# Kernel tuning notes

Measured on AMD Instinct MI355X. Metric: run time of the kernel, lower is better.

Reference implementation:

```python
import jax, jax.numpy as jnp
import numpy as np

B, L, C, H = 4, 2048, 768, 12
D = C // H
MAX_SCALE_MUL = float(np.log(100.0))
BLOCK = 128  # block size for the VAR-style block-causal mask


def _block_causal_bias(L, block):
    # 0 where key-block <= query-block, -inf elsewhere (block lower-triangular)
    bid = np.arange(L) // block
    vis = bid[:, None] >= bid[None, :]
    bias = np.where(vis, 0.0, -np.inf).astype(np.float32)
    return jnp.asarray(bias)[None, None]  # (1,1,L,L)


def setup_inputs() -> dict:
    key = jax.random.key(0)
    ks = jax.random.split(key, 5)
    x = jax.random.normal(ks[0], (B, L, C), dtype=jnp.float32)
    W_qkv = jax.random.normal(ks[1], (3 * C, C), dtype=jnp.float32) * (1.0 / np.sqrt(C))
    q_bias = jnp.zeros((C,), jnp.float32)
    v_bias = jnp.zeros((C,), jnp.float32)
    # module inits scale_mul to log(4.0)
    log_scale_mul = jnp.full((1, H, 1, 1), np.log(4.0), jnp.float32)
    W_proj = jax.random.normal(ks[2], (C, C), dtype=jnp.float32) * (1.0 / np.sqrt(C))
    b_proj = jnp.zeros((C,), jnp.float32)
    attn_bias = _block_causal_bias(L, BLOCK)
    return {"x": x, "attn_bias": attn_bias, "W_qkv": W_qkv, "q_bias": q_bias,
            "v_bias": v_bias, "log_scale_mul": log_scale_mul,
            "W_proj": W_proj, "b_proj": b_proj}


def _l2norm(t, eps=1e-12):
    n = jnp.linalg.norm(t, axis=-1, keepdims=True)
    return t / jnp.maximum(n, eps)


def reference(x, attn_bias, W_qkv, q_bias, v_bias, log_scale_mul, W_proj, b_proj):
    Bx, Lx, Cx = x.shape
    # qkv projection with concatenated (q_bias, zero_k_bias, v_bias)
    bias = jnp.concatenate([q_bias, jnp.zeros_like(q_bias), v_bias])
    qkv = x @ W_qkv.T + bias                      # (B,L,3C)
    qkv = qkv.reshape(Bx, Lx, 3, H, D)
    q, k, v = jnp.moveaxis(qkv, 2, 0)             # each (B,L,H,D)
    q = jnp.swapaxes(q, 1, 2)                     # (B,H,L,D)
    k = jnp.swapaxes(k, 1, 2)
    v = jnp.swapaxes(v, 1, 2)
    # cos-attention: L2-normalize q,k; head-wise learnable scale on q; scale=1
    scale_mul = jnp.exp(jnp.minimum(log_scale_mul, MAX_SCALE_MUL))  # (1,H,1,1)
    q = _l2norm(q) * scale_mul
    k = _l2norm(k)
    scores = jnp.einsum('bhld,bhmd->bhlm', q, k) + attn_bias
    attn = jax.nn.softmax(scores, axis=-1)
    o = jnp.einsum('bhlm,bhmd->bhld', attn, v)    # (B,H,L,D)
    o = jnp.swapaxes(o, 1, 2).reshape(Bx, Lx, Cx)
    return o @ W_proj.T + b_proj
```

## Files before the change

### kernel.cpp

```cpp
#include <hip/hip_runtime.h>
#include <hip/hip_bf16.h>

#define DEV __device__ __forceinline__

typedef __bf16 bf16x8 __attribute__((ext_vector_type(8)));
typedef float  f32x4  __attribute__((ext_vector_type(4)));

typedef __attribute__((address_space(3))) unsigned int LDSU;
typedef __attribute__((address_space(1))) const unsigned int GLBU;

DEV unsigned short f2b(float f){
  __bf16 h = (__bf16)f;
  return __builtin_bit_cast(unsigned short, h);
}

static constexpr float MAXLOG = 4.60517018598809136804f;

__global__ void cvt_kernel(const float4* __restrict__ src, ushort4* __restrict__ dst, int n4){
  int i = blockIdx.x * 256 + threadIdx.x;
  if (i < n4){
    float4 v = src[i];
    ushort4 o;
    o.x = f2b(v.x); o.y = f2b(v.y); o.z = f2b(v.z); o.w = f2b(v.w);
    dst[i] = o;
  }
}

__global__ __launch_bounds__(512) void qkv_gemm(
    const unsigned short* __restrict__ X,
    const unsigned short* __restrict__ W,
    const float* __restrict__ qbias, const float* __restrict__ vbias,
    const float* __restrict__ lsm,
    unsigned short* __restrict__ Qo, unsigned short* __restrict__ Ko,
    unsigned short* __restrict__ Vo)
{
  __shared__ char smem[65536];
  const int tid = threadIdx.x;
  const int l = tid & 63, w = tid >> 6;
  const int wr = w >> 1, wc = w & 1;
  const int lr = l & 15, lg = l >> 4;
  const int tm = blockIdx.x % 64;
  const int tn = blockIdx.x / 64;
  const int m0 = tm * 128, n0 = tn * 128;

  f32x4 acc[2][4];
  #pragma unroll
  for (int i=0;i<2;i++)
    #pragma unroll
    for (int j=0;j<4;j++) acc[i][j] = (f32x4){0.f,0.f,0.f,0.f};

  #pragma unroll
  for (int c=0;c<2;++c){
    int chunk = c*512 + tid;
    int row = chunk >> 3;
    int scc = (chunk & 7) ^ (row & 7);
    __builtin_amdgcn_global_load_lds((GLBU*)(X + (size_t)(m0+row)*768 + scc*8),
                                     (LDSU*)(smem + chunk*16), 16, 0, 0);
    __builtin_amdgcn_global_load_lds((GLBU*)(W + (size_t)(n0+row)*768 + scc*8),
                                     (LDSU*)(smem + 32768 + chunk*16), 16, 0, 0);
  }

  for (int kt = 0; kt < 12; ++kt){
    __syncthreads();
    const int pc = kt & 1;
    char* Acur = smem + pc*16384;
    char* Bcur = smem + 32768 + pc*16384;

    if (kt + 1 < 12){
      const int k1 = (kt+1)*64;
      char* Anxt = smem + (pc^1)*16384;
      char* Bnxt = smem + 32768 + (pc^1)*16384;
      #pragma unroll
      for (int c=0;c<2;++c){
        int chunk = c*512 + tid;
        int row = chunk >> 3;
        int scc = (chunk & 7) ^ (row & 7);
        __builtin_amdgcn_global_load_lds((GLBU*)(X + (size_t)(m0+row)*768 + k1 + scc*8),
                                         (LDSU*)(Anxt + chunk*16), 16, 0, 0);
        __builtin_amdgcn_global_load_lds((GLBU*)(W + (size_t)(n0+row)*768 + k1 + scc*8),
                                         (LDSU*)(Bnxt + chunk*16), 16, 0, 0);
      }
    }

    #pragma unroll
    for (int kk = 0; kk < 2; ++kk){
      bf16x8 af[2], bfv[4];
      #pragma unroll
      for (int m=0;m<2;m++){
        int row = wr*32 + m*16 + lr;
        int byte = kk*64 + lg*16;
        af[m] = *(const bf16x8*)(Acur + row*128 + (byte ^ ((row&7)<<4)));
      }
      #pragma unroll
      for (int n=0;n<4;n++){
        int row = wc*64 + n*16 + lr;
        int byte = kk*64 + lg*16;
        bfv[n] = *(const bf16x8*)(Bcur + row*128 + (byte ^ ((row&7)<<4)));
      }
      #pragma unroll
      for (int m=0;m<2;m++)
        #pragma unroll
        for (int n=0;n<4;n++)
          acc[m][n] = __builtin_amdgcn_mfma_f32_16x16x32_bf16(af[m], bfv[n], acc[m][n], 0, 0, 0);
    }
  }

  const int nb = n0 + wc*64;
  const int seg = nb / 768;
  const int h = (nb % 768) / 64;
  float smul = 1.0f;
  if (seg == 0) smul = __expf(fminf(lsm[h], MAXLOG));
  float bias_v[4];
  #pragma unroll
  for (int n=0;n<4;n++){
    int d = n*16 + lr;
    bias_v[n] = (seg==0) ? qbias[h*64+d] : (seg==2 ? vbias[h*64+d] : 0.f);
  }
  unsigned short* dst = (seg==0) ? Qo : (seg==1 ? Ko : Vo);
  #pragma unroll
  for (int m=0;m<2;m++){
    #pragma unroll
    for (int r=0;r<4;r++){
      float vals[4]; float ss = 0.f;
      #pragma unroll
      for (int n=0;n<4;n++){ float v = acc[m][n][r] + bias_v[n]; vals[n] = v; ss += v*v; }
      ss += __shfl_xor(ss,1); ss += __shfl_xor(ss,2);
      ss += __shfl_xor(ss,4); ss += __shfl_xor(ss,8);
      float sc = (seg==2) ? 1.f : smul / fmaxf(sqrtf(ss), 1e-12f);
      int grow = m0 + wr*32 + m*16 + lg*4 + r;
      int b = grow >> 11, lrow = grow & 2047;
      size_t base = (((size_t)(b*12 + h))*2048 + lrow)*64;
      #pragma unroll
      for (int n=0;n<4;n++) dst[base + n*16 + lr] = f2b(vals[n]*sc);
    }
  }
}

__global__ __launch_bounds__(512) void attn_kernel(
    const unsigned short* __restrict__ Q,
    const unsigned short* __restrict__ K,
    const unsigned short* __restrict__ V,
    const float* __restrict__ lsm,
    unsigned short* __restrict__ O)
{
  __shared__ char smem[49152];
  const int tid = threadIdx.x;
  const int l = tid & 63, w = tid >> 6;
  char* Plds = smem + 32768 + w*2048;
  const int lr = l & 15, lg = l >> 4;

  const int bid = blockIdx.x;
  const int qb = 15 - (bid / 48);
  const int bh = bid % 48;
  const int h = bh % 12;
  const size_t plane = (size_t)bh * (2048*64);
  const int q0 = qb*128 + w*16;

  const float M = __expf(fminf(lsm[h], MAXLOG));

  bf16x8 qf[2];
  #pragma unroll
  for (int ki=0;ki<2;ki++)
    qf[ki] = *(const bf16x8*)(Q + plane + (size_t)(q0 + lr)*64 + ki*32 + lg*8);

  float lsum = 0.f;
  f32x4 of[4];
  #pragma unroll
  for (int di=0;di<4;di++) of[di] = (f32x4){0.f,0.f,0.f,0.f};

  const int krow = tid >> 3;
  const int kscc = (tid & 7) ^ (krow & 7);
  const int rv  = tid & 63;
  const int c0v = (tid >> 6) * 8;

  const int nt = (qb + 1) * 2;

  {
    const unsigned short* Kt0 = K + plane;
    const unsigned short* Vt0 = V + plane;
    __builtin_amdgcn_global_load_lds((GLBU*)(Kt0 + krow*64 + kscc*8),
                                     (LDSU*)(smem + tid*16), 16, 0, 0);
    bf16x8 a = *(const bf16x8*)(Vt0 + rv*64 + c0v);
    #pragma unroll
    for (int j=0;j<8;j++)
      *(__bf16*)(smem + 16384 + (c0v+j)*128 + ((2*rv) ^ (j<<4))) = a[j];
  }

  for (int t = 0; t < nt; ++t){
    __syncthreads();
    const int pc = t & 1;
    char* Kcur = smem + pc*8192;
    char* Vcur = smem + 16384 + pc*8192;
    char* Knxt = smem + (pc^1)*8192;
    char* Vnxt = smem + 16384 + (pc^1)*8192;
    const bool pre = (t+1) < nt;

    bf16x8 nv;
    if (pre){
      const unsigned short* Kt1 = K + plane + (size_t)(t+1)*4096;
      const unsigned short* Vt1 = V + plane + (size_t)(t+1)*4096;
      __builtin_amdgcn_global_load_lds((GLBU*)(Kt1 + krow*64 + kscc*8),
                                       (LDSU*)(Knxt + tid*16), 16, 0, 0);
      nv = *(const bf16x8*)(Vt1 + rv*64 + c0v);
    }

    f32x4 s[4];
    #pragma unroll
    for (int ni=0;ni<4;ni++) s[ni] = (f32x4){0.f,0.f,0.f,0.f};
    #pragma unroll
    for (int ki=0;ki<2;ki++){
      bf16x8 kb[4];
      #pragma unroll
      for (int ni=0;ni<4;ni++){
        int key = ni*16 + lr;
        int byte = ki*64 + lg*16;
        kb[ni] = *(const bf16x8*)(Kcur + key*128 + (byte ^ ((key&7)<<4)));
      }
      #pragma unroll
      for (int ni=0;ni<4;ni++)
        s[ni] = __builtin_amdgcn_mfma_f32_16x16x32_bf16(kb[ni], qf[ki], s[ni], 0, 0, 0);
    }

    {
      const int row = lr;
      float a16 = 0.f;
      #pragma unroll
      for (int ni=0;ni<4;ni++){
        unsigned long long us = 0;
        #pragma unroll
        for (int r=0;r<4;r++){
          float p = __expf(s[ni][r] - M);
          a16 += p;
          us |= ((unsigned long long)f2b(p)) << (16*r);
        }
        *(unsigned long long*)(Plds + row*128 + ((ni*32 + lg*8) ^ ((row&7)<<4))) = us;
      }
      lsum += a16;
    }
    asm volatile("s_waitcnt lgkmcnt(0)" ::: "memory");
    __builtin_amdgcn_sched_barrier(0);

    #pragma unroll
    for (int ki=0;ki<2;ki++){
      bf16x8 pa, vbf[4];
      {
        int row = lr;
        int byte = ki*64 + lg*16;
        pa = *(const bf16x8*)(Plds + row*128 + (byte ^ ((row&7)<<4)));
      }
      #pragma unroll
      for (int di=0;di<4;di++){
        int d = di*16 + lr;
        int byte = ki*64 + lg*16;
        vbf[di] = *(const bf16x8*)(Vcur + d*128 + (byte ^ ((d&7)<<4)));
      }
      #pragma unroll
      for (int di=0;di<4;di++)
        of[di] = __builtin_amdgcn_mfma_f32_16x16x32_bf16(pa, vbf[di], of[di], 0, 0, 0);
    }

    if (pre){
      #pragma unroll
      for (int j=0;j<8;j++)
        *(__bf16*)(Vnxt + (c0v+j)*128 + ((2*rv) ^ (j<<4))) = nv[j];
    }
  }

  {
    float sum = lsum;
    sum += __shfl_xor(sum,16); sum += __shfl_xor(sum,32);
    lsum = sum;
  }
  const int b = bh / 12;
  #pragma unroll
  for (int r=0;r<4;r++){
    float inv = 1.f / __shfl(lsum, lg*4 + r);
    int row = q0 + lg*4 + r;
    size_t base = ((size_t)(b*2048) + row)*768 + h*64;
    #pragma unroll
    for (int di=0;di<4;di++)
      O[base + di*16 + lr] = f2b(of[di][r]*inv);
  }
}

__global__ __launch_bounds__(256) void proj_gemm(
    const unsigned short* __restrict__ A,
    const unsigned short* __restrict__ W,
    const float* __restrict__ bias,
    float* __restrict__ out)
{
  __shared__ char smem[16384];
  char* Alds = smem;
  char* Blds = smem + 8192;

  const int tid = threadIdx.x;
  const int l = tid & 63, w = tid >> 6;
  const int lr = l & 15, lg = l >> 4;
  const int tm = blockIdx.x % 128;
  const int tn = blockIdx.x / 128;
  const int m0 = tm * 64, n0 = tn * 64;

  f32x4 acc[4];
  #pragma unroll
  for (int j=0;j<4;j++) acc[j] = (f32x4){0.f,0.f,0.f,0.f};

  for (int kt = 0; kt < 12; ++kt){
    const int k0 = kt * 64;
    __syncthreads();
    #pragma unroll
    for (int c = 0; c < 2; ++c){
      int chunk = c*256 + tid;
      int row = chunk >> 3;
      int scc = (chunk & 7) ^ (row & 7);
      __builtin_amdgcn_global_load_lds((GLBU*)(A + (size_t)(m0+row)*768 + k0 + scc*8),
                                       (LDSU*)(Alds + (c*256 + w*64)*16), 16, 0, 0);
      __builtin_amdgcn_global_load_lds((GLBU*)(W + (size_t)(n0+row)*768 + k0 + scc*8),
                                       (LDSU*)(Blds + (c*256 + w*64)*16), 16, 0, 0);
    }
    __syncthreads();
    #pragma unroll
    for (int kk = 0; kk < 2; ++kk){
      bf16x8 af, bfv[4];
      {
        int row = w*16 + lr;
        int byte = kk*64 + lg*16;
        af = *(const bf16x8*)(Alds + row*128 + (byte ^ ((row&7)<<4)));
      }
      #pragma unroll
      for (int n=0;n<4;n++){
        int row = n*16 + lr;
        int byte = kk*64 + lg*16;
        bfv[n] = *(const bf16x8*)(Blds + row*128 + (byte ^ ((row&7)<<4)));
      }
      #pragma unroll
      for (int n=0;n<4;n++)
        acc[n] = __builtin_amdgcn_mfma_f32_16x16x32_bf16(af, bfv[n], acc[n], 0, 0, 0);
    }
  }

  #pragma unroll
  for (int r=0;r<4;r++){
    int grow = m0 + w*16 + lg*4 + r;
    #pragma unroll
    for (int n=0;n<4;n++){
      int colg = n0 + n*16 + lr;
      out[(size_t)grow*768 + colg] = acc[n][r] + bias[colg];
    }
  }
}

extern "C" void kernel_launch(void* const* d_in, const int* in_sizes, int n_in,
                              void* d_out, int out_size, void* d_ws, size_t ws_size,
                              hipStream_t stream)
{
  const float* x     = (const float*)d_in[0];
  const float* Wqkv  = (const float*)d_in[2];
  const float* qbias = (const float*)d_in[3];
  const float* vbias = (const float*)d_in[4];
  const float* lsm   = (const float*)d_in[5];
  const float* Wproj = (const float*)d_in[6];
  const float* bproj = (const float*)d_in[7];
  float* out = (float*)d_out;

  char* ws = (char*)d_ws;
  size_t off = 0;
  auto alloc = [&](size_t bytes)->char*{
    char* p = ws + off; off += (bytes + 255) & ~(size_t)255; return p;
  };
  unsigned short* xb  = (unsigned short*)alloc((size_t)8192*768*2);
  unsigned short* wqb = (unsigned short*)alloc((size_t)2304*768*2);
  unsigned short* wpb = (unsigned short*)alloc((size_t)768*768*2);
  unsigned short* qn  = (unsigned short*)alloc((size_t)48*2048*64*2);
  unsigned short* kn  = (unsigned short*)alloc((size_t)48*2048*64*2);
  unsigned short* vn  = (unsigned short*)alloc((size_t)48*2048*64*2);
  unsigned short* ob  = (unsigned short*)alloc((size_t)8192*768*2);

  cvt_kernel<<<6144, 256, 0, stream>>>((const float4*)x,     (ushort4*)xb,  1572864);
  cvt_kernel<<<1728, 256, 0, stream>>>((const float4*)Wqkv,  (ushort4*)wqb,  442368);
  cvt_kernel<<< 576, 256, 0, stream>>>((const float4*)Wproj, (ushort4*)wpb,  147456);
  qkv_gemm<<<64*18, 512, 0, stream>>>(xb, wqb, qbias, vbias, lsm, qn, kn, vn);
  attn_kernel<<<768, 512, 0, stream>>>(qn, kn, vn, lsm, ob);
  proj_gemm<<<128*12, 256, 0, stream>>>(ob, wpb, bproj, out);
}
```

Measured before the change: 129.1 us.

## Split long attention query blocks across two KV halves with atomic combine

Query blocks 8–15, which scan the most key tiles, are each split into two work items covering half the key range. The extra 384 blocks even out per-block work and shorten the tail of the attention launch. Their unnormalized fp32 outputs and row sums are accumulated with atomics into a scratch buffer placed over the bf16 x area, which qkv_gemm has already consumed. A new combine kernel then normalizes those rows into bf16. The cost is an extra memset, atomic traffic, and a second small kernel launch.

Result: slower. 155.2 us (+20.3%).

```diff
diff --git a/kernel.cpp b/kernel.cpp
--- a/kernel.cpp
+++ b/kernel.cpp
@@ -141,7 +141,9 @@
     const unsigned short* __restrict__ K,
     const unsigned short* __restrict__ V,
     const float* __restrict__ lsm,
-    unsigned short* __restrict__ O)
+    unsigned short* __restrict__ O,
+    float* __restrict__ part,
+    float* __restrict__ plsum)
 {
   __shared__ char smem[49152];
   const int tid = threadIdx.x;
@@ -150,8 +152,12 @@
   const int lr = l & 15, lg = l >> 4;
 
   const int bid = blockIdx.x;
-  const int qb = 15 - (bid / 48);
+  const int u  = bid / 48;
   const int bh = bid % 48;
+  int qb, t0, cnt; bool split;
+  if (u < 16){ qb = 15 - (u >> 1); cnt = qb + 1; t0 = (u & 1) * cnt; split = true; }
+  else       { qb = 23 - u;        cnt = (qb + 1) * 2; t0 = 0;       split = false; }
+
   const int h = bh % 12;
   const size_t plane = (size_t)bh * (2048*64);
   const int q0 = qb*128 + w*16;
@@ -173,11 +179,9 @@
   const int rv  = tid & 63;
   const int c0v = (tid >> 6) * 8;
 
-  const int nt = (qb + 1) * 2;
-
   {
-    const unsigned short* Kt0 = K + plane;
-    const unsigned short* Vt0 = V + plane;
+    const unsigned short* Kt0 = K + plane + (size_t)t0*4096;
+    const unsigned short* Vt0 = V + plane + (size_t)t0*4096;
     __builtin_amdgcn_global_load_lds((GLBU*)(Kt0 + krow*64 + kscc*8),
                                      (LDSU*)(smem + tid*16), 16, 0, 0);
     bf16x8 a = *(const bf16x8*)(Vt0 + rv*64 + c0v);
@@ -186,19 +190,19 @@
       *(__bf16*)(smem + 16384 + (c0v+j)*128 + ((2*rv) ^ (j<<4))) = a[j];
   }
 
-  for (int t = 0; t < nt; ++t){
+  for (int tt = 0; tt < cnt; ++tt){
     __syncthreads();
-    const int pc = t & 1;
+    const int pc = tt & 1;
     char* Kcur = smem + pc*8192;
     char* Vcur = smem + 16384 + pc*8192;
     char* Knxt = smem + (pc^1)*8192;
     char* Vnxt = smem + 16384 + (pc^1)*8192;
-    const bool pre = (t+1) < nt;
+    const bool pre = (tt+1) < cnt;
 
     bf16x8 nv;
     if (pre){
-      const unsigned short* Kt1 = K + plane + (size_t)(t+1)*4096;
-      const unsigned short* Vt1 = V + plane + (size_t)(t+1)*4096;
+      const unsigned short* Kt1 = K + plane + (size_t)(t0+tt+1)*4096;
+      const unsigned short* Vt1 = V + plane + (size_t)(t0+tt+1)*4096;
       __builtin_amdgcn_global_load_lds((GLBU*)(Kt1 + krow*64 + kscc*8),
                                        (LDSU*)(Knxt + tid*16), 16, 0, 0);
       nv = *(const bf16x8*)(Vt1 + rv*64 + c0v);
@@ -266,21 +270,47 @@
     }
   }
 
-  {
-    float sum = lsum;
-    sum += __shfl_xor(sum,16); sum += __shfl_xor(sum,32);
-    lsum = sum;
-  }
-  const int b = bh / 12;
-  #pragma unroll
-  for (int r=0;r<4;r++){
-    float inv = 1.f / __shfl(lsum, lg*4 + r);
-    int row = q0 + lg*4 + r;
-    size_t base = ((size_t)(b*2048) + row)*768 + h*64;
-    #pragma unroll
-    for (int di=0;di<4;di++)
-      O[base + di*16 + lr] = f2b(of[di][r]*inv);
-  }
+  float sum = lsum;
+  sum += __shfl_xor(sum,16); sum += __shfl_xor(sum,32);
+
+  if (!split){
+    const int b = bh / 12;
+    #pragma unroll
+    for (int r=0;r<4;r++){
+      float inv = 1.f / __shfl(sum, lg*4 + r);
+      int row = q0 + lg*4 + r;
+      size_t base = ((size_t)(b*2048) + row)*768 + h*64;
+      #pragma unroll
+      for (int di=0;di<4;di++)
+        O[base + di*16 + lr] = f2b(of[di][r]*inv);
+    }
+  } else {
+    const int sb = ((qb-8)*48 + bh)*128 + w*16;
+    #pragma unroll
+    for (int r=0;r<4;r++){
+      float rowsum = __shfl(sum, lg*4 + r);
+      int srow = sb + lg*4 + r;
+      if (lr == 0) atomicAdd(&plsum[srow], rowsum);
+      #pragma unroll
+      for (int di=0;di<4;di++)
+        atomicAdd(&part[(size_t)srow*64 + di*16 + lr], of[di][r]);
+    }
+  }
+}
+
+__global__ __launch_bounds__(256) void combine_kernel(
+    const float* __restrict__ part, const float* __restrict__ plsum,
+    unsigned short* __restrict__ O)
+{
+  int i = blockIdx.x * 256 + threadIdx.x;
+  int srow = i >> 6, d = i & 63;
+  int qb8 = srow / 6144;
+  int rem = srow % 6144;
+  int bh = rem >> 7, lrow = rem & 127;
+  int qrow = (qb8 + 8)*128 + lrow;
+  int b = bh / 12, h = bh % 12;
+  O[((size_t)b*2048 + qrow)*768 + h*64 + d] =
+      f2b(part[(size_t)srow*64 + d] / plsum[srow]);
 }
 
 __global__ __launch_bounds__(256) void proj_gemm(
@@ -375,10 +405,15 @@
   unsigned short* vn  = (unsigned short*)alloc((size_t)48*2048*64*2);
   unsigned short* ob  = (unsigned short*)alloc((size_t)8192*768*2);
 
+  float* part  = (float*)xb;
+  float* plsum = part + (size_t)49152*64;
+
   cvt_kernel<<<6144, 256, 0, stream>>>((const float4*)x,     (ushort4*)xb,  1572864);
   cvt_kernel<<<1728, 256, 0, stream>>>((const float4*)Wqkv,  (ushort4*)wqb,  442368);
   cvt_kernel<<< 576, 256, 0, stream>>>((const float4*)Wproj, (ushort4*)wpb,  147456);
   qkv_gemm<<<64*18, 512, 0, stream>>>(xb, wqb, qbias, vbias, lsm, qn, kn, vn);
-  attn_kernel<<<768, 512, 0, stream>>>(qn, kn, vn, lsm, ob);
+  hipMemsetAsync(part, 0, (size_t)49152*65*4, stream);
+  attn_kernel<<<1152, 512, 0, stream>>>(qn, kn, vn, lsm, ob, part, plsum);
+  combine_kernel<<<12288, 256, 0, stream>>>(part, plsum, ob);
   proj_gemm<<<128*12, 256, 0, stream>>>(ob, wpb, bproj, out);
 }
```
